# Performance work log

Measured on AMD Instinct MI355X. Metric: run time of the kernel, lower is better.

Reference implementation:

```python
import jax, jax.numpy as jnp
import numpy as np

D_MODEL = 1024
N_HEADS = 16
D_FF = 4096
LN_EPS = 1e-5


def _layer_norm(x, g, b):
    m = jnp.mean(x, axis=-1, keepdims=True)
    v = jnp.mean((x - m) ** 2, axis=-1, keepdims=True)
    return (x - m) / jnp.sqrt(v + LN_EPS) * g + b


def setup_inputs() -> dict:
    key = jax.random.key(0)
    ks = jax.random.split(key, 16)
    s = 0.02
    d, dff = D_MODEL, D_FF
    return {
        "x": jax.random.normal(ks[0], (8, 1000, d), dtype=jnp.float32),
        # weights stored as (d_in, d_out); applied via x @ W
        "wq": jax.random.normal(ks[1], (d, d), dtype=jnp.float32) * s,
        "wk": jax.random.normal(ks[2], (d, d), dtype=jnp.float32) * s,
        "wv": jax.random.normal(ks[3], (d, d), dtype=jnp.float32) * s,
        "wo": jax.random.normal(ks[4], (d, d), dtype=jnp.float32) * s,
        "bo": jnp.zeros((d,), dtype=jnp.float32),
        "w1": jax.random.normal(ks[5], (d, dff), dtype=jnp.float32) * s,
        "b1": jnp.zeros((dff,), dtype=jnp.float32),
        "w2": jax.random.normal(ks[6], (dff, d), dtype=jnp.float32) * s,
        "b2": jnp.zeros((d,), dtype=jnp.float32),
        "g1": jnp.ones((d,), dtype=jnp.float32),
        "beta1": jnp.zeros((d,), dtype=jnp.float32),
        "g2": jnp.ones((d,), dtype=jnp.float32),
        "beta2": jnp.zeros((d,), dtype=jnp.float32),
    }


def reference(x, wq, wk, wv, wo, bo, w1, b1, w2, b2, g1, beta1, g2, beta2):
    B, S, D = x.shape
    H = N_HEADS
    dk = D // H

    # --- pre-norm attention ---
    h = _layer_norm(x, g1, beta1)
    q = (h @ wq).reshape(B, S, H, dk)
    k = (h @ wk).reshape(B, S, H, dk)
    v = (h @ wv).reshape(B, S, H, dk)
    scores = jnp.einsum('bqhd,bkhd->bhqk', q, k) / jnp.sqrt(jnp.float32(dk))
    mask = jnp.tril(jnp.ones((S, S), dtype=bool))  # causal
    scores = jnp.where(mask, scores, -jnp.inf)
    attn = jax.nn.softmax(scores, axis=-1)
    attended = jnp.einsum('bhqk,bkhd->bqhd', attn, v).reshape(B, S, D)
    x = x + attended @ wo + bo

    # --- pre-norm FFN (exact GELU, matching torch F.gelu default) ---
    h2 = _layer_norm(x, g2, beta2)
    ff = jax.nn.gelu(h2 @ w1 + b1, approximate=False) @ w2 + b2
    return x + ff
```

## Files before the change

kernel.cpp:

```cpp
#include <hip/hip_runtime.h>
#include <hip/hip_bf16.h>
#include <math.h>

#define D_MODEL 1024
#define D_FF    4096
#define N_HEADS 16
#define SEQ     1000
#define BATCH   8
#define M_TOK   (BATCH * SEQ)

typedef __bf16 bf16x8_t __attribute__((ext_vector_type(8)));
typedef short  short8_t __attribute__((ext_vector_type(8)));
typedef float  f32x4_t  __attribute__((ext_vector_type(4)));

__device__ __forceinline__ f32x4_t mfma_bf16(short8_t a, short8_t b, f32x4_t c) {
    return __builtin_amdgcn_mfma_f32_16x16x32_bf16(
        __builtin_bit_cast(bf16x8_t, a), __builtin_bit_cast(bf16x8_t, b), c, 0, 0, 0);
}

__device__ __forceinline__ unsigned short f2bf(float f) {
    union { float f; unsigned u; } x; x.f = f;
    unsigned r = (x.u + 0x7fffu + ((x.u >> 16) & 1u)) >> 16;
    return (unsigned short)r;
}

__device__ __forceinline__ float gelu_fast(float v) {
    float z = 1.5957691216f * v * fmaf(0.044715f, v * v, 1.0f);
    float e = __expf(-z);
    return v * __builtin_amdgcn_rcpf(1.0f + e);
}

__device__ __forceinline__ void gload_lds16(const void* g, void* l) {
    __builtin_amdgcn_global_load_lds(
        (const __attribute__((address_space(1))) unsigned int*)g,
        (__attribute__((address_space(3))) unsigned int*)l, 16, 0, 0);
}

__global__ __launch_bounds__(256) void prep_kernel(
    const float* __restrict__ wq, const float* __restrict__ wk,
    const float* __restrict__ wv, const float* __restrict__ wo,
    const float* __restrict__ w1, const float* __restrict__ w2,
    unsigned short* __restrict__ wqt, unsigned short* __restrict__ wkt,
    unsigned short* __restrict__ wvt, unsigned short* __restrict__ wot,
    unsigned short* __restrict__ w1t, unsigned short* __restrict__ w2t,
    const float* __restrict__ x, const float* __restrict__ g1,
    const float* __restrict__ beta1, unsigned short* __restrict__ h1) {
    int id = blockIdx.x;
    __shared__ float tile[32][33];
    __shared__ float red[8];
    if (id >= 12288) {
        int row = id - 12288, tid = threadIdx.x;
        const float4 v = ((const float4*)(x + (size_t)row * D_MODEL))[tid];
        float s  = v.x + v.y + v.z + v.w;
        float s2 = v.x * v.x + v.y * v.y + v.z * v.z + v.w * v.w;
#pragma unroll
        for (int o = 32; o > 0; o >>= 1) { s += __shfl_xor(s, o, 64); s2 += __shfl_xor(s2, o, 64); }
        int wave = tid >> 6, lane = tid & 63;
        if (lane == 0) { red[wave] = s; red[wave + 4] = s2; }
        __syncthreads();
        s  = red[0] + red[1] + red[2] + red[3];
        s2 = red[4] + red[5] + red[6] + red[7];
        float mean = s * (1.0f / D_MODEL);
        float var  = s2 * (1.0f / D_MODEL) - mean * mean;
        float rstd = rsqrtf(var + 1e-5f);
        float4 gg = ((const float4*)g1)[tid];
        float4 bb = ((const float4*)beta1)[tid];
        ushort4 o4;
        o4.x = f2bf((v.x - mean) * rstd * gg.x + bb.x);
        o4.y = f2bf((v.y - mean) * rstd * gg.y + bb.y);
        o4.z = f2bf((v.z - mean) * rstd * gg.z + bb.z);
        o4.w = f2bf((v.w - mean) * rstd * gg.w + bb.w);
        ((ushort4*)(h1 + (size_t)row * D_MODEL))[tid] = o4;
        return;
    }
    const float* w; unsigned short* wt; int Kd, Nd, bx, by;
    if (id < 4096) {
        int z = id >> 10, t = id & 1023;
        w  = z == 0 ? wq  : z == 1 ? wk  : z == 2 ? wv  : wo;
        wt = z == 0 ? wqt : z == 1 ? wkt : z == 2 ? wvt : wot;
        Kd = 1024; Nd = 1024; bx = t & 31; by = t >> 5;
    } else if (id < 8192) {
        int t = id - 4096;
        w = w1; wt = w1t; Kd = 1024; Nd = 4096; bx = t & 127; by = t >> 7;
    } else {
        int t = id - 8192;
        w = w2; wt = w2t; Kd = 4096; Nd = 1024; bx = t & 31; by = t >> 5;
    }
    int n0 = bx * 32, k0 = by * 32;
    int tx = threadIdx.x & 31, ty = threadIdx.x >> 5;
#pragma unroll
    for (int i = 0; i < 4; ++i)
        tile[ty + i * 8][tx] = w[(size_t)(k0 + ty + i * 8) * Nd + n0 + tx];
    __syncthreads();
#pragma unroll
    for (int i = 0; i < 4; ++i)
        wt[(size_t)(n0 + ty + i * 8) * Kd + k0 + tx] = f2bf(tile[tx][ty + i * 8]);
}

__global__ __launch_bounds__(256) void vtrans_kernel(const unsigned short* __restrict__ v,
                                                     unsigned short* __restrict__ vt) {
    __shared__ unsigned short tile[32][33];
    int b = blockIdx.z;
    int c0 = blockIdx.x * 32, s0 = blockIdx.y * 32;
    int tx = threadIdx.x, ty = threadIdx.y;
#pragma unroll
    for (int i = 0; i < 4; ++i) {
        int s = s0 + ty + i * 8;
        unsigned short val = 0;
        if (s < SEQ) val = v[((size_t)b * SEQ + s) * D_MODEL + c0 + tx];
        tile[ty + i * 8][tx] = val;
    }
    __syncthreads();
#pragma unroll
    for (int i = 0; i < 4; ++i) {
        int c = c0 + ty + i * 8;
        vt[((size_t)b * D_MODEL + c) * 1024 + s0 + tx] = tile[tx][ty + i * 8];
    }
}

__global__ __launch_bounds__(256) void ln_kernel(const float* __restrict__ x,
                                                 const float* __restrict__ g,
                                                 const float* __restrict__ beta,
                                                 unsigned short* __restrict__ out) {
    int row = blockIdx.x, tid = threadIdx.x;
    const float4 v = ((const float4*)(x + (size_t)row * D_MODEL))[tid];
    float s  = v.x + v.y + v.z + v.w;
    float s2 = v.x * v.x + v.y * v.y + v.z * v.z + v.w * v.w;
#pragma unroll
    for (int o = 32; o > 0; o >>= 1) { s += __shfl_xor(s, o, 64); s2 += __shfl_xor(s2, o, 64); }
    __shared__ float red[8];
    int wave = tid >> 6, lane = tid & 63;
    if (lane == 0) { red[wave] = s; red[wave + 4] = s2; }
    __syncthreads();
    s  = red[0] + red[1] + red[2] + red[3];
    s2 = red[4] + red[5] + red[6] + red[7];
    float mean = s * (1.0f / D_MODEL);
    float var  = s2 * (1.0f / D_MODEL) - mean * mean;
    float rstd = rsqrtf(var + 1e-5f);
    float4 gg = ((const float4*)g)[tid];
    float4 bb = ((const float4*)beta)[tid];
    ushort4 o4;
    o4.x = f2bf((v.x - mean) * rstd * gg.x + bb.x);
    o4.y = f2bf((v.y - mean) * rstd * gg.y + bb.y);
    o4.z = f2bf((v.z - mean) * rstd * gg.z + bb.z);
    o4.w = f2bf((v.w - mean) * rstd * gg.w + bb.w);
    ((ushort4*)(out + (size_t)row * D_MODEL))[tid] = o4;
}

enum { EPI_BF16 = 0, EPI_GELU = 1, EPI_RES_F32 = 2 };

template <int EPI, int KDIM, bool FUSE3>
__global__ __launch_bounds__(256) void gemm_bt(
    const unsigned short* __restrict__ A,
    const unsigned short* __restrict__ Bt0,
    const unsigned short* __restrict__ Bt1,
    const unsigned short* __restrict__ Bt2,
    const float* __restrict__ bias,
    const float* __restrict__ resid,
    void* __restrict__ out0, void* out1, void* out2,
    int Mdim, int Ndim) {
    constexpr int K = KDIM;
    constexpr int NKT = K / 64;
    __shared__ unsigned short lda[2][128 * 64];
    __shared__ unsigned short ldb[2][128 * 64];
    int tid = threadIdx.x;
    int lane = tid & 63, wave = tid >> 6;
    int l15 = lane & 15, quad = lane >> 4;
    int rt = blockIdx.y * 128;
    const unsigned short* Bt = Bt0;
    void* outp = out0;
    int ct;
    if (FUSE3) {
        int sel = blockIdx.x >> 3;
        ct = (blockIdx.x & 7) * 128;
        Bt   = sel == 0 ? Bt0  : (sel == 1 ? Bt1  : Bt2);
        outp = sel == 0 ? out0 : (sel == 1 ? out1 : out2);
    } else {
        ct = blockIdx.x * 128;
    }
    int wr = (wave >> 1) * 64, wc = (wave & 1) * 64;
    f32x4_t acc[4][4] = {};

    const unsigned short* ag[4];
    const unsigned short* bg[4];
#pragma unroll
    for (int i = 0; i < 4; ++i) {
        int gidx = tid + i * 256;
        int row = gidx >> 3, cp = gidx & 7;
        int c = cp ^ (row & 7);
        int ar = rt + row; if (ar >= Mdim) ar = Mdim - 1;
        ag[i] = A  + (size_t)ar * K + c * 8;
        bg[i] = Bt + (size_t)(ct + row) * K + c * 8;
    }

    auto stage = [&](int kt, int bufi) {
#pragma unroll
        for (int i = 0; i < 4; ++i) {
            gload_lds16(ag[i] + kt * 64, (char*)lda[bufi] + (wave * 64 + i * 256) * 16);
            gload_lds16(bg[i] + kt * 64, (char*)ldb[bufi] + (wave * 64 + i * 256) * 16);
        }
    };

    stage(0, 0);
    for (int kt = 0; kt < NKT; ++kt) {
        int bufi = kt & 1;
        __syncthreads();
        if (kt + 1 < NKT) stage(kt + 1, bufi ^ 1);
        const unsigned short* la = lda[bufi];
        const unsigned short* lb = ldb[bufi];
#pragma unroll
        for (int kc = 0; kc < 2; ++kc) {
            short8_t af[4], bfr[4];
#pragma unroll
            for (int mi = 0; mi < 4; ++mi) {
                int ra = wr + mi * 16 + l15;
                int cg = (kc * 4 + quad) ^ (ra & 7);
                af[mi] = *(const short8_t*)(la + (ra * 8 + cg) * 8);
            }
#pragma unroll
            for (int ni = 0; ni < 4; ++ni) {
                int rb = wc + ni * 16 + l15;
                int cg = (kc * 4 + quad) ^ (rb & 7);
                bfr[ni] = *(const short8_t*)(lb + (rb * 8 + cg) * 8);
            }
#pragma unroll
            for (int mi = 0; mi < 4; ++mi)
#pragma unroll
                for (int ni = 0; ni < 4; ++ni)
                    acc[mi][ni] = mfma_bf16(af[mi], bfr[ni], acc[mi][ni]);
        }
    }

    float bias_c[4];
    if (EPI != EPI_BF16) {
#pragma unroll
        for (int ni = 0; ni < 4; ++ni) bias_c[ni] = bias[ct + wc + ni * 16 + l15];
    }

#pragma unroll
    for (int mi = 0; mi < 4; ++mi) {
#pragma unroll
        for (int r = 0; r < 4; ++r) {
            int grow = rt + wr + mi * 16 + quad * 4 + r;
            if (grow >= Mdim) continue;
#pragma unroll
            for (int ni = 0; ni < 4; ++ni) {
                int gcol = ct + wc + ni * 16 + l15;
                float v = acc[mi][ni][r];
                size_t idx = (size_t)grow * Ndim + gcol;
                if (EPI == EPI_BF16) {
                    ((unsigned short*)outp)[idx] = f2bf(v);
                } else if (EPI == EPI_GELU) {
                    v += bias_c[ni];
                    ((unsigned short*)outp)[idx] = f2bf(gelu_fast(v));
                } else {
                    v += bias_c[ni] + resid[idx];
                    ((float*)outp)[idx] = v;
                }
            }
        }
    }
}

template <int EPI, bool FUSE3>
__global__ __launch_bounds__(512, 2) void gemm256(
    const unsigned short* __restrict__ A,
    const unsigned short* __restrict__ Bt0,
    const unsigned short* __restrict__ Bt1,
    const unsigned short* __restrict__ Bt2,
    const float* __restrict__ bias,
    const float* __restrict__ resid,
    void* __restrict__ out0, void* out1, void* out2,
    int Mdim, int Ndim, int K) {
    __shared__ unsigned short lds[4][2][256 * 32];
    int tid = threadIdx.x;
    int lane = tid & 63, wave = tid >> 6;
    int l15 = lane & 15, quad = lane >> 4;
    int wr = wave >> 2;
    int wc = wave & 3;
    int rt = blockIdx.y * 256;
    const unsigned short* Bt = Bt0;
    void* outp = out0;
    int ct;
    if (FUSE3) {
        int sel = blockIdx.x >> 2;
        ct = (blockIdx.x & 3) * 256;
        Bt   = sel == 0 ? Bt0  : (sel == 1 ? Bt1  : Bt2);
        outp = sel == 0 ? out0 : (sel == 1 ? out1 : out2);
    } else {
        ct = blockIdx.x * 256;
    }

    const unsigned short* aS[2];
    const unsigned short* bS[2];
#pragma unroll
    for (int j = 0; j < 2; ++j) {
        int gl = tid + j * 512;
        int p = gl >> 3, slot = gl & 7;
        int sp = slot ^ (p & 7);
        int rrow = 2 * p + (sp >> 2), g2 = sp & 3;
        int ar = rt + rrow; if (ar >= Mdim) ar = Mdim - 1;
        aS[j] = A  + (size_t)ar * K + g2 * 8;
        bS[j] = Bt + (size_t)(ct + rrow) * K + g2 * 8;
    }
    auto stageA = [&](int kt) {
        char* base = (char*)&lds[kt & 3][0][0];
#pragma unroll
        for (int j = 0; j < 2; ++j)
            gload_lds16(aS[j] + (size_t)kt * 32, base + (wave * 64 + j * 512) * 16);
    };
    auto stageB = [&](int kt) {
        char* base = (char*)&lds[kt & 3][1][0];
#pragma unroll
        for (int j = 0; j < 2; ++j)
            gload_lds16(bS[j] + (size_t)kt * 32, base + (wave * 64 + j * 512) * 16);
    };

    int lh = l15 >> 1;
    int mslot = (quad + ((l15 & 1) << 2)) ^ lh;
    unsigned aOff = (unsigned)((wr * 64 + lh) * 128 + mslot * 16);
    unsigned bOff = (unsigned)((wc * 32 + lh) * 128 + mslot * 16);

    f32x4_t acc[8][4] = {};
    int NT = K >> 5;

    stageA(0); stageB(0); stageA(1); stageB(1); stageA(2); stageB(2);

    for (int t = 0; t < NT; ++t) {
        int sl = t & 3;
        asm volatile("s_waitcnt vmcnt(8)" ::: "memory");
        __builtin_amdgcn_s_barrier();
        const char* la = (const char*)&lds[sl][0][0];
        const char* lb = (const char*)&lds[sl][1][0];
        short8_t af[4], bfv[4];
#pragma unroll
        for (int mi = 0; mi < 4; ++mi)
            af[mi] = *(const short8_t*)(la + aOff + mi * 1024);
#pragma unroll
        for (int ni = 0; ni < 4; ++ni)
            bfv[ni] = *(const short8_t*)(lb + bOff + ni * 1024);
        if (t + 3 < NT) stageA(t + 3);
        __builtin_amdgcn_s_setprio(1);
#pragma unroll
        for (int mi = 0; mi < 4; ++mi)
#pragma unroll
            for (int ni = 0; ni < 4; ++ni)
                acc[mi][ni] = mfma_bf16(af[mi], bfv[ni], acc[mi][ni]);
        __builtin_amdgcn_s_setprio(0);
        asm volatile("" ::: "memory");
        __builtin_amdgcn_s_barrier();
#pragma unroll
        for (int mi = 0; mi < 4; ++mi)
            af[mi] = *(const short8_t*)(la + aOff + 4096 + mi * 1024);
        if (t + 3 < NT) stageB(t + 3);
        __builtin_amdgcn_s_setprio(1);
#pragma unroll
        for (int mi = 0; mi < 4; ++mi)
#pragma unroll
            for (int ni = 0; ni < 4; ++ni)
                acc[4 + mi][ni] = mfma_bf16(af[mi], bfv[ni], acc[4 + mi][ni]);
        __builtin_amdgcn_s_setprio(0);
    }

    float bias_c[4];
    if (EPI != EPI_BF16) {
#pragma unroll
        for (int ni = 0; ni < 4; ++ni) bias_c[ni] = bias[ct + wc * 64 + ni * 16 + l15];
    }

#pragma unroll
    for (int mi = 0; mi < 8; ++mi) {
#pragma unroll
        for (int r = 0; r < 4; ++r) {
            int grow = rt + wr * 128 + mi * 16 + quad * 4 + r;
            if (grow >= Mdim) continue;
#pragma unroll
            for (int ni = 0; ni < 4; ++ni) {
                int gcol = ct + wc * 64 + ni * 16 + l15;
                float v = acc[mi][ni][r];
                size_t idx = (size_t)grow * Ndim + gcol;
                if (EPI == EPI_BF16) {
                    ((unsigned short*)outp)[idx] = f2bf(v);
                } else if (EPI == EPI_GELU) {
                    v += bias_c[ni];
                    ((unsigned short*)outp)[idx] = f2bf(gelu_fast(v));
                } else {
                    v += bias_c[ni] + resid[idx];
                    ((float*)outp)[idx] = v;
                }
            }
        }
    }
}

__global__ __launch_bounds__(256) void attn_kernel(
    const unsigned short* __restrict__ q,
    const unsigned short* __restrict__ k,
    const unsigned short* __restrict__ vt,
    unsigned short* __restrict__ att) {
    int p = blockIdx.x, h = blockIdx.y, b = blockIdx.z;
    int tid = threadIdx.x, lane = tid & 63, wave = tid >> 6;
    int l15 = lane & 15, quad = lane >> 4;
    __shared__ unsigned short kt_lds[2][64 * 64];
    __shared__ unsigned short vt_lds[2][64 * 64];
    __shared__ unsigned short p_lds[4][32 * 64];
    unsigned short* pw = p_lds[wave];

    const int qtA = p, qtB = 7 - p;
    const int tA = 2 * qtA + 2, tB = 2 * qtB + 2, total = tA + tB;

    short8_t aq[2][2][2];
#pragma unroll
    for (int ph = 0; ph < 2; ++ph) {
        int qw = (ph ? qtB : qtA) * 128 + wave * 32;
#pragma unroll
        for (int g = 0; g < 2; ++g) {
            int qr = qw + g * 16 + l15; if (qr > SEQ - 1) qr = SEQ - 1;
            const unsigned short* qp = q + ((size_t)(b * SEQ + qr)) * D_MODEL + h * 64 + quad * 8;
            aq[ph][g][0] = *(const short8_t*)qp;
            aq[ph][g][1] = *(const short8_t*)(qp + 32);
        }
    }

    f32x4_t o[2][4] = {};
    float m_run[2] = {-3.0e38f, -3.0e38f};
    float l_run[2] = {0.f, 0.f};

    auto stage = [&](int kt, int bufi) {
#pragma unroll
        for (int i = 0; i < 2; ++i) {
            int g2 = tid + i * 256;
            int row = g2 >> 3, cp = g2 & 7;
            int c = cp ^ (row & 7);
            int key = kt * 64 + row; int keyc = key < SEQ ? key : SEQ - 1;
            gload_lds16(k + ((size_t)(b * SEQ + keyc)) * D_MODEL + h * 64 + c * 8,
                        (char*)kt_lds[bufi] + (size_t)(wave * 64 + i * 256) * 16);
            gload_lds16(vt + ((size_t)((b * N_HEADS + h) * 64 + row)) * 1024 + kt * 64 + c * 8,
                        (char*)vt_lds[bufi] + (size_t)(wave * 64 + i * 256) * 16);
        }
    };

    auto flush = [&](int qt) {
#pragma unroll
        for (int g = 0; g < 2; ++g) {
            float linv = __builtin_amdgcn_rcpf(l_run[g]);
#pragma unroll
            for (int r = 0; r < 4; ++r) {
                float nr = __shfl(linv, quad * 4 + r, 64);
                int qg = qt * 128 + wave * 32 + g * 16 + quad * 4 + r;
                if (qg >= SEQ) continue;
#pragma unroll
                for (int db = 0; db < 4; ++db)
                    att[((size_t)(b * SEQ + qg)) * D_MODEL + h * 64 + db * 16 + l15] =
                        f2bf(o[g][db][r] * nr);
            }
        }
#pragma unroll
        for (int g = 0; g < 2; ++g) {
            m_run[g] = -3.0e38f; l_run[g] = 0.f;
#pragma unroll
            for (int db = 0; db < 4; ++db) o[g][db] = f32x4_t{0.f, 0.f, 0.f, 0.f};
        }
    };

    stage(0, 0);

    for (int i = 0; i < total; ++i) {
        int bufi = i & 1;
        __syncthreads();
        if (i + 1 < total) {
            int nkt = (i + 1 < tA) ? (i + 1) : (i + 1 - tA);
            stage(nkt, bufi ^ 1);
        }
        int phase = (i < tA) ? 0 : 1;
        int kt = (i < tA) ? i : i - tA;
        int qt = phase ? qtB : qtA;
        int qw = qt * 128 + wave * 32;
        const unsigned short* kl = kt_lds[bufi];
        const unsigned short* vl = vt_lds[bufi];

        if (kt * 64 <= qw + 31) {
            short8_t kf[4][2];
#pragma unroll
            for (int nb = 0; nb < 4; ++nb)
#pragma unroll
                for (int kc = 0; kc < 2; ++kc) {
                    int row = nb * 16 + l15;
                    kf[nb][kc] = *(const short8_t*)(kl + (row * 8 + ((kc * 4 + quad) ^ (row & 7))) * 8);
                }

            bool gact[2];
#pragma unroll
            for (int g = 0; g < 2; ++g) {
                gact[g] = (kt * 64 <= qw + g * 16 + 15);
                if (!gact[g]) continue;
                f32x4_t s[4] = {};
#pragma unroll
                for (int nb = 0; nb < 4; ++nb)
#pragma unroll
                    for (int kc = 0; kc < 2; ++kc)
                        s[nb] = mfma_bf16(kf[nb][kc], aq[phase][g][kc], s[nb]);
                int qrow = qw + g * 16 + l15;
                float sc[4][4];
#pragma unroll
                for (int nb = 0; nb < 4; ++nb)
#pragma unroll
                    for (int r = 0; r < 4; ++r) {
                        int key = kt * 64 + nb * 16 + quad * 4 + r;
                        float v = s[nb][r] * 0.125f;
                        sc[nb][r] = (key <= qrow) ? v : -1e30f;
                    }
                float mx = sc[0][0];
#pragma unroll
                for (int nb = 0; nb < 4; ++nb)
#pragma unroll
                    for (int r = 0; r < 4; ++r) mx = fmaxf(mx, sc[nb][r]);
                mx = fmaxf(mx, __shfl_xor(mx, 16, 64));
                mx = fmaxf(mx, __shfl_xor(mx, 32, 64));
                float mnew = fmaxf(m_run[g], mx);
                float alpha = __expf(m_run[g] - mnew);
                m_run[g] = mnew;
                float rs = 0.f;
#pragma unroll
                for (int nb = 0; nb < 4; ++nb)
#pragma unroll
                    for (int r = 0; r < 4; ++r) {
                        float pv = __expf(sc[nb][r] - mnew);
                        sc[nb][r] = pv;
                        rs += pv;
                    }
                rs += __shfl_xor(rs, 16, 64);
                rs += __shfl_xor(rs, 32, 64);
                l_run[g] = l_run[g] * alpha + rs;
#pragma unroll
                for (int r = 0; r < 4; ++r) {
                    float a = __shfl(alpha, quad * 4 + r, 64);
#pragma unroll
                    for (int db = 0; db < 4; ++db) o[g][db][r] *= a;
                }
#pragma unroll
                for (int nb = 0; nb < 4; ++nb) {
                    unsigned long long pv =
                        (unsigned long long)f2bf(sc[nb][0]) |
                        ((unsigned long long)f2bf(sc[nb][1]) << 16) |
                        ((unsigned long long)f2bf(sc[nb][2]) << 32) |
                        ((unsigned long long)f2bf(sc[nb][3]) << 48);
                    int chunk = (4 * nb + quad) ^ ((l15 & 7) << 1);
                    *(unsigned long long*)(pw + (g * 16 + l15) * 64 + chunk * 4) = pv;
                }
            }
            asm volatile("s_waitcnt lgkmcnt(0)" ::: "memory");

            short8_t vf[4][2];
#pragma unroll
            for (int db = 0; db < 4; ++db)
#pragma unroll
                for (int kc = 0; kc < 2; ++kc) {
                    int row = db * 16 + l15;
                    vf[db][kc] = *(const short8_t*)(vl + (row * 8 + ((kc * 4 + quad) ^ (row & 7))) * 8);
                }
#pragma unroll
            for (int g = 0; g < 2; ++g) {
                if (!gact[g]) continue;
                short8_t ap[2];
#pragma unroll
                for (int kc = 0; kc < 2; ++kc)
                    ap[kc] = *(const short8_t*)(pw + (g * 16 + l15) * 64 +
                                                ((kc * 4 + quad) ^ (l15 & 7)) * 8);
#pragma unroll
                for (int db = 0; db < 4; ++db)
#pragma unroll
                    for (int kc = 0; kc < 2; ++kc)
                        o[g][db] = mfma_bf16(ap[kc], vf[db][kc], o[g][db]);
            }
        }

        if (i == tA - 1) flush(qtA);
    }
    flush(qtB);
}

extern "C" void kernel_launch(void* const* d_in, const int* in_sizes, int n_in,
                              void* d_out, int out_size, void* d_ws, size_t ws_size,
                              hipStream_t stream) {
    const float* x     = (const float*)d_in[0];
    const float* wq    = (const float*)d_in[1];
    const float* wk    = (const float*)d_in[2];
    const float* wv    = (const float*)d_in[3];
    const float* wo    = (const float*)d_in[4];
    const float* bo    = (const float*)d_in[5];
    const float* w1    = (const float*)d_in[6];
    const float* b1    = (const float*)d_in[7];
    const float* w2    = (const float*)d_in[8];
    const float* b2    = (const float*)d_in[9];
    const float* g1    = (const float*)d_in[10];
    const float* beta1 = (const float*)d_in[11];
    const float* g2    = (const float*)d_in[12];
    const float* beta2 = (const float*)d_in[13];
    float* out = (float*)d_out;
    char* ws = (char*)d_ws;

    const size_t SZ_MD_BF16 = (size_t)M_TOK * D_MODEL * 2;
    unsigned short* h1  = (unsigned short*)(ws);
    unsigned short* qb  = (unsigned short*)(ws + SZ_MD_BF16);
    unsigned short* kb  = (unsigned short*)(ws + 2 * SZ_MD_BF16);
    unsigned short* vb  = (unsigned short*)(ws + 3 * SZ_MD_BF16);
    unsigned short* atb = (unsigned short*)(ws + 4 * SZ_MD_BF16);
    unsigned short* ffb = qb;
    size_t off = 5 * SZ_MD_BF16;
    unsigned short* vtb = (unsigned short*)(ws + off); off += (size_t)BATCH * D_MODEL * 1024 * 2;
    float* x1 = (float*)(ws + off); off += (size_t)M_TOK * D_MODEL * 4;
    unsigned short* wqt = (unsigned short*)(ws + off); off += (size_t)D_MODEL * D_MODEL * 2;
    unsigned short* wkt = (unsigned short*)(ws + off); off += (size_t)D_MODEL * D_MODEL * 2;
    unsigned short* wvt = (unsigned short*)(ws + off); off += (size_t)D_MODEL * D_MODEL * 2;
    unsigned short* wot = (unsigned short*)(ws + off); off += (size_t)D_MODEL * D_MODEL * 2;
    unsigned short* w1t = (unsigned short*)(ws + off); off += (size_t)D_MODEL * D_FF * 2;
    unsigned short* w2t = (unsigned short*)(ws + off); off += (size_t)D_MODEL * D_FF * 2;

    prep_kernel<<<12288 + M_TOK, 256, 0, stream>>>(
        wq, wk, wv, wo, w1, w2, wqt, wkt, wvt, wot, w1t, w2t, x, g1, beta1, h1);

    const int MT128 = (M_TOK + 127) / 128;
    const int MT256 = (M_TOK + 255) / 256;

    gemm256<EPI_BF16, true><<<dim3(12, MT256), 512, 0, stream>>>(
        h1, wqt, wkt, wvt, nullptr, nullptr, qb, kb, vb, M_TOK, D_MODEL, D_MODEL);

    dim3 tb(32, 8);
    vtrans_kernel<<<dim3(32, 32, 8), tb, 0, stream>>>(vb, vtb);

    attn_kernel<<<dim3(4, N_HEADS, BATCH), 256, 0, stream>>>(qb, kb, vtb, atb);

    gemm_bt<EPI_RES_F32, D_MODEL, false><<<dim3(8, MT128), 256, 0, stream>>>(
        atb, wot, nullptr, nullptr, bo, x, x1, nullptr, nullptr, M_TOK, D_MODEL);

    ln_kernel<<<M_TOK, 256, 0, stream>>>(x1, g2, beta2, h1);

    gemm256<EPI_GELU, false><<<dim3(16, MT256), 512, 0, stream>>>(
        h1, w1t, nullptr, nullptr, b1, nullptr, ffb, nullptr, nullptr, M_TOK, D_FF, D_MODEL);

    gemm256<EPI_RES_F32, false><<<dim3(4, MT256), 512, 0, stream>>>(
        ffb, w2t, nullptr, nullptr, b2, x1, out, nullptr, nullptr, M_TOK, D_MODEL, D_FF);
}
```

Baseline: 504.3 us.

## Add 128x256-tile GEMM and use it for QKV, output projection and FFN2

Adds a gemm128 kernel with 128x256 output tiles, 8 waves and a 4-stage global-to-LDS pipeline. QKV, Wo and W2 GEMMs now use it instead of the 256x256 and old 128x128 kernels. The smaller M tile doubles the block count for N=1024 GEMMs, which should give better CU fill on MI355X (256 CUs). It also makes the vmcnt wait tail-aware so the last iterations wait on exactly the loads still outstanding. Each block gets less operand reuse per loaded byte.

```diff
diff --git a/kernel.cpp b/kernel.cpp
--- a/kernel.cpp
+++ b/kernel.cpp
@@ -148,119 +148,6 @@
 }
 
 enum { EPI_BF16 = 0, EPI_GELU = 1, EPI_RES_F32 = 2 };
-
-template <int EPI, int KDIM, bool FUSE3>
-__global__ __launch_bounds__(256) void gemm_bt(
-    const unsigned short* __restrict__ A,
-    const unsigned short* __restrict__ Bt0,
-    const unsigned short* __restrict__ Bt1,
-    const unsigned short* __restrict__ Bt2,
-    const float* __restrict__ bias,
-    const float* __restrict__ resid,
-    void* __restrict__ out0, void* out1, void* out2,
-    int Mdim, int Ndim) {
-    constexpr int K = KDIM;
-    constexpr int NKT = K / 64;
-    __shared__ unsigned short lda[2][128 * 64];
-    __shared__ unsigned short ldb[2][128 * 64];
-    int tid = threadIdx.x;
-    int lane = tid & 63, wave = tid >> 6;
-    int l15 = lane & 15, quad = lane >> 4;
-    int rt = blockIdx.y * 128;
-    const unsigned short* Bt = Bt0;
-    void* outp = out0;
-    int ct;
-    if (FUSE3) {
-        int sel = blockIdx.x >> 3;
-        ct = (blockIdx.x & 7) * 128;
-        Bt   = sel == 0 ? Bt0  : (sel == 1 ? Bt1  : Bt2);
-        outp = sel == 0 ? out0 : (sel == 1 ? out1 : out2);
-    } else {
-        ct = blockIdx.x * 128;
-    }
-    int wr = (wave >> 1) * 64, wc = (wave & 1) * 64;
-    f32x4_t acc[4][4] = {};
-
-    const unsigned short* ag[4];
-    const unsigned short* bg[4];
-#pragma unroll
-    for (int i = 0; i < 4; ++i) {
-        int gidx = tid + i * 256;
-        int row = gidx >> 3, cp = gidx & 7;
-        int c = cp ^ (row & 7);
-        int ar = rt + row; if (ar >= Mdim) ar = Mdim - 1;
-        ag[i] = A  + (size_t)ar * K + c * 8;
-        bg[i] = Bt + (size_t)(ct + row) * K + c * 8;
-    }
-
-    auto stage = [&](int kt, int bufi) {
-#pragma unroll
-        for (int i = 0; i < 4; ++i) {
-            gload_lds16(ag[i] + kt * 64, (char*)lda[bufi] + (wave * 64 + i * 256) * 16);
-            gload_lds16(bg[i] + kt * 64, (char*)ldb[bufi] + (wave * 64 + i * 256) * 16);
-        }
-    };
-
-    stage(0, 0);
-    for (int kt = 0; kt < NKT; ++kt) {
-        int bufi = kt & 1;
-        __syncthreads();
-        if (kt + 1 < NKT) stage(kt + 1, bufi ^ 1);
-        const unsigned short* la = lda[bufi];
-        const unsigned short* lb = ldb[bufi];
-#pragma unroll
-        for (int kc = 0; kc < 2; ++kc) {
-            short8_t af[4], bfr[4];
-#pragma unroll
-            for (int mi = 0; mi < 4; ++mi) {
-                int ra = wr + mi * 16 + l15;
-                int cg = (kc * 4 + quad) ^ (ra & 7);
-                af[mi] = *(const short8_t*)(la + (ra * 8 + cg) * 8);
-            }
-#pragma unroll
-            for (int ni = 0; ni < 4; ++ni) {
-                int rb = wc + ni * 16 + l15;
-                int cg = (kc * 4 + quad) ^ (rb & 7);
-                bfr[ni] = *(const short8_t*)(lb + (rb * 8 + cg) * 8);
-            }
-#pragma unroll
-            for (int mi = 0; mi < 4; ++mi)
-#pragma unroll
-                for (int ni = 0; ni < 4; ++ni)
-                    acc[mi][ni] = mfma_bf16(af[mi], bfr[ni], acc[mi][ni]);
-        }
-    }
-
-    float bias_c[4];
-    if (EPI != EPI_BF16) {
-#pragma unroll
-        for (int ni = 0; ni < 4; ++ni) bias_c[ni] = bias[ct + wc + ni * 16 + l15];
-    }
-
-#pragma unroll
-    for (int mi = 0; mi < 4; ++mi) {
-#pragma unroll
-        for (int r = 0; r < 4; ++r) {
-            int grow = rt + wr + mi * 16 + quad * 4 + r;
-            if (grow >= Mdim) continue;
-#pragma unroll
-            for (int ni = 0; ni < 4; ++ni) {
-                int gcol = ct + wc + ni * 16 + l15;
-                float v = acc[mi][ni][r];
-                size_t idx = (size_t)grow * Ndim + gcol;
-                if (EPI == EPI_BF16) {
-                    ((unsigned short*)outp)[idx] = f2bf(v);
-                } else if (EPI == EPI_GELU) {
-                    v += bias_c[ni];
-                    ((unsigned short*)outp)[idx] = f2bf(gelu_fast(v));
-                } else {
-                    v += bias_c[ni] + resid[idx];
-                    ((float*)outp)[idx] = v;
-                }
-            }
-        }
-    }
-}
 
 template <int EPI, bool FUSE3>
 __global__ __launch_bounds__(512, 2) void gemm256(
@@ -328,7 +215,10 @@
 
     for (int t = 0; t < NT; ++t) {
         int sl = t & 3;
-        asm volatile("s_waitcnt vmcnt(8)" ::: "memory");
+        int rem = NT - 1 - t;
+        if (rem >= 2)      asm volatile("s_waitcnt vmcnt(8)" ::: "memory");
+        else if (rem == 1) asm volatile("s_waitcnt vmcnt(4)" ::: "memory");
+        else               asm volatile("s_waitcnt vmcnt(0)" ::: "memory");
         __builtin_amdgcn_s_barrier();
         const char* la = (const char*)&lds[sl][0][0];
         const char* lb = (const char*)&lds[sl][1][0];
@@ -373,6 +263,125 @@
 #pragma unroll
         for (int r = 0; r < 4; ++r) {
             int grow = rt + wr * 128 + mi * 16 + quad * 4 + r;
+            if (grow >= Mdim) continue;
+#pragma unroll
+            for (int ni = 0; ni < 4; ++ni) {
+                int gcol = ct + wc * 64 + ni * 16 + l15;
+                float v = acc[mi][ni][r];
+                size_t idx = (size_t)grow * Ndim + gcol;
+                if (EPI == EPI_BF16) {
+                    ((unsigned short*)outp)[idx] = f2bf(v);
+                } else if (EPI == EPI_GELU) {
+                    v += bias_c[ni];
+                    ((unsigned short*)outp)[idx] = f2bf(gelu_fast(v));
+                } else {
+                    v += bias_c[ni] + resid[idx];
+                    ((float*)outp)[idx] = v;
+                }
+            }
+        }
+    }
+}
+
+template <int EPI, bool FUSE3>
+__global__ __launch_bounds__(512, 2) void gemm128(
+    const unsigned short* __restrict__ A,
+    const unsigned short* __restrict__ Bt0,
+    const unsigned short* __restrict__ Bt1,
+    const unsigned short* __restrict__ Bt2,
+    const float* __restrict__ bias,
+    const float* __restrict__ resid,
+    void* __restrict__ out0, void* out1, void* out2,
+    int Mdim, int Ndim, int K) {
+    __shared__ unsigned short ldsA[4][128 * 32];
+    __shared__ unsigned short ldsB[4][256 * 32];
+    int tid = threadIdx.x;
+    int lane = tid & 63, wave = tid >> 6;
+    int l15 = lane & 15, quad = lane >> 4;
+    int wr = wave >> 2;
+    int wc = wave & 3;
+    int rt = blockIdx.y * 128;
+    const unsigned short* Bt = Bt0;
+    void* outp = out0;
+    int ct;
+    if (FUSE3) {
+        int sel = blockIdx.x >> 2;
+        ct = (blockIdx.x & 3) * 256;
+        Bt   = sel == 0 ? Bt0  : (sel == 1 ? Bt1  : Bt2);
+        outp = sel == 0 ? out0 : (sel == 1 ? out1 : out2);
+    } else {
+        ct = blockIdx.x * 256;
+    }
+
+    const unsigned short* aSrc;
+    {
+        int p = tid >> 3, sp = (tid & 7) ^ (p & 7);
+        int rrow = 2 * p + (sp >> 2), g2 = sp & 3;
+        int ar = rt + rrow; if (ar >= Mdim) ar = Mdim - 1;
+        aSrc = A + (size_t)ar * K + g2 * 8;
+    }
+    const unsigned short* bSrc[2];
+#pragma unroll
+    for (int j = 0; j < 2; ++j) {
+        int gl = tid + j * 512;
+        int p = gl >> 3, sp = (gl & 7) ^ (p & 7);
+        int rrow = 2 * p + (sp >> 2), g2 = sp & 3;
+        bSrc[j] = Bt + (size_t)(ct + rrow) * K + g2 * 8;
+    }
+    auto stage = [&](int kt) {
+        int sl = kt & 3;
+        gload_lds16(aSrc + (size_t)kt * 32, (char*)ldsA[sl] + wave * 1024);
+        gload_lds16(bSrc[0] + (size_t)kt * 32, (char*)ldsB[sl] + wave * 1024);
+        gload_lds16(bSrc[1] + (size_t)kt * 32, (char*)ldsB[sl] + 8192 + wave * 1024);
+    };
+
+    int lh = l15 >> 1;
+    int mslot = (quad + ((l15 & 1) << 2)) ^ lh;
+    unsigned aOff = (unsigned)((wr * 32 + lh) * 128 + mslot * 16);
+    unsigned bOff = (unsigned)((wc * 32 + lh) * 128 + mslot * 16);
+
+    f32x4_t acc[4][4] = {};
+    int NT = K >> 5;
+
+    stage(0); stage(1); stage(2);
+
+    for (int t = 0; t < NT; ++t) {
+        int sl = t & 3;
+        int rem = NT - 1 - t;
+        if (rem >= 2)      asm volatile("s_waitcnt vmcnt(6)" ::: "memory");
+        else if (rem == 1) asm volatile("s_waitcnt vmcnt(3)" ::: "memory");
+        else               asm volatile("s_waitcnt vmcnt(0)" ::: "memory");
+        __builtin_amdgcn_s_barrier();
+        const char* la = (const char*)ldsA[sl];
+        const char* lb = (const char*)ldsB[sl];
+        short8_t af[4], bfv[4];
+#pragma unroll
+        for (int mi = 0; mi < 4; ++mi)
+            af[mi] = *(const short8_t*)(la + aOff + mi * 1024);
+#pragma unroll
+        for (int ni = 0; ni < 4; ++ni)
+            bfv[ni] = *(const short8_t*)(lb + bOff + ni * 1024);
+        if (t + 3 < NT) stage(t + 3);
+        __builtin_amdgcn_s_setprio(1);
+#pragma unroll
+        for (int mi = 0; mi < 4; ++mi)
+#pragma unroll
+            for (int ni = 0; ni < 4; ++ni)
+                acc[mi][ni] = mfma_bf16(af[mi], bfv[ni], acc[mi][ni]);
+        __builtin_amdgcn_s_setprio(0);
+    }
+
+    float bias_c[4];
+    if (EPI != EPI_BF16) {
+#pragma unroll
+        for (int ni = 0; ni < 4; ++ni) bias_c[ni] = bias[ct + wc * 64 + ni * 16 + l15];
+    }
+
+#pragma unroll
+    for (int mi = 0; mi < 4; ++mi) {
+#pragma unroll
+        for (int r = 0; r < 4; ++r) {
+            int grow = rt + wr * 64 + mi * 16 + quad * 4 + r;
             if (grow >= Mdim) continue;
 #pragma unroll
             for (int ni = 0; ni < 4; ++ni) {
@@ -623,7 +632,7 @@
     const int MT128 = (M_TOK + 127) / 128;
     const int MT256 = (M_TOK + 255) / 256;
 
-    gemm256<EPI_BF16, true><<<dim3(12, MT256), 512, 0, stream>>>(
+    gemm128<EPI_BF16, true><<<dim3(12, MT128), 512, 0, stream>>>(
         h1, wqt, wkt, wvt, nullptr, nullptr, qb, kb, vb, M_TOK, D_MODEL, D_MODEL);
 
     dim3 tb(32, 8);
@@ -631,14 +640,14 @@
 
     attn_kernel<<<dim3(4, N_HEADS, BATCH), 256, 0, stream>>>(qb, kb, vtb, atb);
 
-    gemm_bt<EPI_RES_F32, D_MODEL, false><<<dim3(8, MT128), 256, 0, stream>>>(
-        atb, wot, nullptr, nullptr, bo, x, x1, nullptr, nullptr, M_TOK, D_MODEL);
+    gemm128<EPI_RES_F32, false><<<dim3(4, MT128), 512, 0, stream>>>(
+        atb, wot, nullptr, nullptr, bo, x, x1, nullptr, nullptr, M_TOK, D_MODEL, D_MODEL);
 
     ln_kernel<<<M_TOK, 256, 0, stream>>>(x1, g2, beta2, h1);
 
     gemm256<EPI_GELU, false><<<dim3(16, MT256), 512, 0, stream>>>(
         h1, w1t, nullptr, nullptr, b1, nullptr, ffb, nullptr, nullptr, M_TOK, D_FF, D_MODEL);
 
-    gemm256<EPI_RES_F32, false><<<dim3(4, MT256), 512, 0, stream>>>(
+    gemm128<EPI_RES_F32, false><<<dim3(4, MT128), 512, 0, stream>>>(
         ffb, w2t, nullptr, nullptr, b2, x1, out, nullptr, nullptr, M_TOK, D_MODEL, D_FF);
 }
```

Result: faster. 477.4 us (-5.3%).
